# Performance work log

Measured on AMD Instinct MI355X. Metric: run time of the kernel, lower is better.

## Reference

```python
import jax, jax.numpy as jnp
import numpy as np

# Static configuration (mirrors init_kwargs)
B, C, H, W = 4, 256, 128, 128
S, T = 512, 64          # style_dim, num style tokens
HC, HS = 4, 8           # cross-attn heads, spatial-attn heads
WS, G = 8, 4            # window size, groupnorm groups
SHARPEN = 2.0
EPS = 1e-5


def _ln(x, g, b):
    m = jnp.mean(x, -1, keepdims=True)
    v = jnp.var(x, -1, keepdims=True)
    return (x - m) * jax.lax.rsqrt(v + EPS) * g + b


def _sdpa(q, k, v, scale):
    # q,k,v: [B, nH, L, D]
    s = jnp.einsum('bhqd,bhkd->bhqk', q, k) * scale
    return jnp.einsum('bhqk,bhkd->bhqd', jax.nn.softmax(s, -1), v)


def _heads(t, nh):
    b, l, c = t.shape
    return t.reshape(b, l, nh, c // nh).transpose(0, 2, 1, 3)


def _unheads(t):
    b, nh, l, d = t.shape
    return t.transpose(0, 2, 1, 3).reshape(b, l, nh * d)


def setup_inputs() -> dict:
    key = jax.random.key(0)
    ks = iter(jax.random.split(key, 48))
    def w(shape, s=0.02):
        return jax.random.normal(next(ks), shape, jnp.float32) * s
    return {
        'x': jax.random.normal(next(ks), (B, C, H, W), jnp.float32),
        'style_code': jax.random.normal(next(ks), (B, S), jnp.float32),
        # SpatialSelfAttention params (1x1 convs == linear over channels)
        'qkv_w': w((3 * C, C)), 'spat_proj_w': w((C, C)),
        # CrossAttnAdaGN params
        'gproj_w': w((2 * C, S)),
        'gproj_b': jnp.concatenate([jnp.ones((C,), jnp.float32), jnp.zeros((C,), jnp.float32)]),
        'tokens_basis': w((T, C)),
        'sproj_w': w((C, S)), 'sproj_b': jnp.zeros((C,), jnp.float32),
        'pos_w1': w((C, 2)), 'pos_b1': jnp.zeros((C,), jnp.float32),
        'pos_w2': w((C, C)), 'pos_b2': jnp.zeros((C,), jnp.float32),
        'q_w': w((C, C)), 'q_b': jnp.zeros((C,), jnp.float32),
        'k_w': w((C, C)), 'k_b': jnp.zeros((C,), jnp.float32),
        'v_w': w((C, C)), 'v_b': jnp.zeros((C,), jnp.float32),
        'o_w': w((C, C)), 'o_b': jnp.zeros((C,), jnp.float32),
        'ffn_w1': w((2 * C, C)), 'ffn_b1': jnp.zeros((2 * C,), jnp.float32),
        'ffn_w2': w((C, 2 * C)), 'ffn_b2': jnp.zeros((C,), jnp.float32),
        'tn_g': jnp.ones((C,), jnp.float32), 'tn_b': jnp.zeros((C,), jnp.float32),
        'qn_g': jnp.ones((C,), jnp.float32), 'qn_b': jnp.zeros((C,), jnp.float32),
        'fn_g': jnp.ones((C,), jnp.float32), 'fn_b': jnp.zeros((C,), jnp.float32),
        'gamma': w((1, C, 1, 1), 0.1),
    }


def reference(x, style_code, qkv_w, spat_proj_w, gproj_w, gproj_b, tokens_basis,
              sproj_w, sproj_b, pos_w1, pos_b1, pos_w2, pos_b2,
              q_w, q_b, k_w, k_b, v_w, v_b, o_w, o_b,
              ffn_w1, ffn_b1, ffn_w2, ffn_b2,
              tn_g, tn_b, qn_g, qn_b, fn_g, fn_b, gamma):
    b = x.shape[0]
    hw = H * W
    # ---------- CrossAttnAdaGN style modulation ----------
    xg = x.reshape(b, G, C // G, H, W)
    mu = jnp.mean(xg, (2, 3, 4), keepdims=True)
    var = jnp.var(xg, (2, 3, 4), keepdims=True)
    normalized = ((xg - mu) * jax.lax.rsqrt(var + EPS)).reshape(b, C, H, W)
    gp = style_code @ gproj_w.T + gproj_b           # [B, 2C]
    scale = gp[:, :C, None, None]
    shift = gp[:, C:, None, None]
    style_tokens = tokens_basis[None] + (style_code @ sproj_w.T + sproj_b)[:, None]  # [B,T,C]
    style_tokens = _ln(style_tokens, tn_g, tn_b)
    gy = jnp.linspace(-1.0, 1.0, H)
    gx = jnp.linspace(-1.0, 1.0, W)
    grid_y, grid_x = jnp.meshgrid(gy, gx, indexing='ij')
    pos = jnp.stack([grid_x, grid_y], -1).reshape(hw, 2)                 # [HW,2]
    pos_emb = jax.nn.silu(pos @ pos_w1.T + pos_b1) @ pos_w2.T + pos_b2   # [HW,C]
    tok = normalized.transpose(0, 2, 3, 1).reshape(b, hw, C)
    q_in = _ln(tok + pos_emb[None], qn_g, qn_b)
    q = _heads(q_in @ q_w.T + q_b, HC)                 # [B,HC,HW,hd]
    k = _heads(style_tokens @ k_w.T + k_b, HC)         # [B,HC,T,hd]
    v = _heads(style_tokens @ v_w.T + v_b, HC)
    hd = C // HC
    sc = _unheads(_sdpa(q, k, v, SHARPEN / jnp.sqrt(jnp.float32(hd))))   # [B,HW,C]
    sc = sc @ o_w.T + o_b
    sc = sc + jax.nn.silu(_ln(sc, fn_g, fn_b) @ ffn_w1.T + ffn_b1) @ ffn_w2.T + ffn_b2
    sc_sp = sc.transpose(0, 2, 1).reshape(b, C, H, W)
    adagn = normalized * scale + shift + sc_sp * gamma
    h = x + adagn  # gate = 1.0, residual style modulation
    # ---------- shifted-window self-attention ----------
    sh = WS // 2
    xr = jnp.roll(h, (-sh, -sh), (2, 3))
    qkv = jnp.einsum('oi,bihw->bohw', qkv_w, xr)
    qs, ks_, vs = jnp.split(qkv, 3, axis=1)
    def win(t):  # [B,C,H,W] -> [B*nWin, WS*WS, C]
        return t.reshape(b, C, H // WS, WS, W // WS, WS).transpose(0, 2, 4, 3, 5, 1).reshape(-1, WS * WS, C)
    hd2 = C // HS
    qh = _heads(win(qs), HS)
    kh = _heads(win(ks_), HS)
    vh = _heads(win(vs), HS)
    out = _unheads(_sdpa(qh, kh, vh, 1.0 / jnp.sqrt(jnp.float32(hd2))))
    out = out.reshape(b, H // WS, W // WS, WS, WS, C).transpose(0, 5, 1, 3, 2, 4).reshape(b, C, H, W)
    out = jnp.roll(out, (sh, sh), (2, 3))
    out = jnp.einsum('oi,bihw->bohw', spat_proj_w, out)
    return h + out
```

## Files before the change

### kernel.cpp

```cpp
#include <hip/hip_runtime.h>
#include <stdint.h>

#define DEV __device__ __forceinline__

typedef unsigned short u16;
typedef unsigned int u32;
typedef __attribute__((ext_vector_type(8))) __bf16 bf16x8;
typedef __attribute__((ext_vector_type(4))) float f32x4;

DEV u16 f2b(float f) {
  u32 u = __float_as_uint(f);
  u32 r = (u + 0x7FFFu + ((u >> 16) & 1u)) >> 16;
  return (u16)r;
}
DEV float b2f(u16 u) { return __uint_as_float(((u32)u) << 16); }
DEV void up2(u32 u, float& a, float& b) {
  a = __uint_as_float(u << 16);
  b = __uint_as_float(u & 0xffff0000u);
}
DEV void up8(uint4 t, float* d) {
  up2(t.x, d[0], d[1]); up2(t.y, d[2], d[3]);
  up2(t.z, d[4], d[5]); up2(t.w, d[6], d[7]);
}
DEV float silu_f(float v) { return v / (1.0f + __expf(-v)); }

DEV float redmax16(float v) {
  v = fmaxf(v, __shfl_xor(v, 1));
  v = fmaxf(v, __shfl_xor(v, 2));
  v = fmaxf(v, __shfl_xor(v, 4));
  v = fmaxf(v, __shfl_xor(v, 8));
  return v;
}
DEV float redsum16(float v) {
  v += __shfl_xor(v, 1);
  v += __shfl_xor(v, 2);
  v += __shfl_xor(v, 4);
  v += __shfl_xor(v, 8);
  return v;
}

DEV void gload16(const u16* g, u16* l) {
  __builtin_amdgcn_global_load_lds(
      (const __attribute__((address_space(1))) uint32_t*)(g),
      (__attribute__((address_space(3))) uint32_t*)(l), 16, 0, 0);
}

struct WConv {
  const float* s0; const float* s1; const float* s2; const float* s3;
  const float* s4; const float* s5; const float* s6;
  u16* d0; u16* d1; u16* d2; u16* d3; u16* d4; u16* d5; u16* d6;
};
__global__ void k_conv_all(WConv wc) {
  int i = blockIdx.x * 256 + threadIdx.x;
  if (i >= 180224) return;
  const float* sp[7] = {wc.s0, wc.s1, wc.s2, wc.s3, wc.s4, wc.s5, wc.s6};
  u16* dp[7] = {wc.d0, wc.d1, wc.d2, wc.d3, wc.d4, wc.d5, wc.d6};
  const int n4[7] = {16384, 16384, 32768, 32768, 49152, 16384, 16384};
  int rem = i, seg = 0;
#pragma unroll
  for (int s = 0; s < 7; ++s) {
    if (rem < n4[s]) { seg = s; break; }
    rem -= n4[s];
  }
  float4 v = ((const float4*)sp[seg])[rem];
  u16 t[4] = {f2b(v.x), f2b(v.y), f2b(v.z), f2b(v.w)};
  *(uint2*)(dp[seg] + (rem << 2)) = *(uint2*)t;
}

DEV void breduce2(float& a, float& b, float* red, int tid) {
#pragma unroll
  for (int off = 32; off > 0; off >>= 1) {
    a += __shfl_down(a, off);
    b += __shfl_down(b, off);
  }
  int lane = tid & 63, wv = tid >> 6;
  if (lane == 0) { red[wv * 2] = a; red[wv * 2 + 1] = b; }
  __syncthreads();
  a = red[0] + red[2] + red[4] + red[6];
  b = red[1] + red[3] + red[5] + red[7];
}

template <int XB>
__global__ void k_gn_partial(const float* __restrict__ x, float* __restrict__ partials,
                             u16* __restrict__ xb) {
  __shared__ float red[8];
  int chunk = blockIdx.x;
  size_t base4 = ((size_t)chunk) << 12;
  const float4* x4 = (const float4*)x;
  float a = 0.f, b = 0.f;
#pragma unroll 4
  for (int i = 0; i < 16; ++i) {
    size_t idx = base4 + (i << 8) + threadIdx.x;
    float4 v = x4[idx];
    a += v.x + v.y + v.z + v.w;
    b += v.x * v.x + v.y * v.y + v.z * v.z + v.w * v.w;
    if (XB) {
      u16 t[4] = {f2b(v.x), f2b(v.y), f2b(v.z), f2b(v.w)};
      *(uint2*)(xb + (idx << 2)) = *(uint2*)t;
    }
  }
  breduce2(a, b, red, threadIdx.x);
  if (threadIdx.x == 0) { partials[chunk * 2] = a; partials[chunk * 2 + 1] = b; }
}

__global__ void k_gn_final(const float* __restrict__ partials, float* __restrict__ stats) {
  int g = blockIdx.x, lane = threadIdx.x;
  float a = partials[(((g << 6) + lane) << 1)];
  float b = partials[(((g << 6) + lane) << 1) + 1];
#pragma unroll
  for (int off = 32; off > 0; off >>= 1) {
    a += __shfl_down(a, off);
    b += __shfl_down(b, off);
  }
  if (lane == 0) {
    float mean = a * (1.f / 1048576.f);
    float var = b * (1.f / 1048576.f) - mean * mean;
    stats[g << 1] = mean;
    stats[(g << 1) + 1] = rsqrtf(var + 1e-5f);
  }
}

__global__ void k_style(const float* __restrict__ sc, const float* __restrict__ gw,
                        const float* __restrict__ gb, const float* __restrict__ sw,
                        const float* __restrict__ sb, float* __restrict__ gp,
                        float* __restrict__ stok) {
  __shared__ float row[512];
  int b = blockIdx.y, part = blockIdx.x, tid = threadIdx.x;
  row[tid] = sc[(b << 9) + tid];
  row[tid + 256] = sc[(b << 9) + tid + 256];
  __syncthreads();
  if (part < 2) {
    int o = (part << 8) + tid;
    float s = gb[o];
    const float* wr = gw + ((size_t)o << 9);
#pragma unroll 8
    for (int j = 0; j < 512; ++j) s += row[j] * wr[j];
    gp[(b << 9) + o] = s;
  } else {
    float s = sb[tid];
    const float* wr = sw + ((size_t)tid << 9);
#pragma unroll 8
    for (int j = 0; j < 512; ++j) s += row[j] * wr[j];
    stok[(b << 8) + tid] = s;
  }
}

__global__ void k_styk(const float* __restrict__ tb, const float* __restrict__ stok,
                       const float* __restrict__ g, const float* __restrict__ bt,
                       float* __restrict__ styk) {
  __shared__ float red[8];
  int r = blockIdx.x;
  int b = r >> 6, t = r & 63;
  int c = threadIdx.x;
  float v = tb[(t << 8) + c] + stok[(b << 8) + c];
  float a = v, bb = v * v;
  breduce2(a, bb, red, c);
  float mean = a * (1.f / 256.f);
  float var = bb * (1.f / 256.f) - mean * mean;
  float rs = rsqrtf(var + 1e-5f);
  styk[((size_t)r << 8) + c] = (v - mean) * rs * g[c] + bt[c];
}

__global__ void k_kv(const float* __restrict__ styk, const float* __restrict__ kw,
                     const float* __restrict__ kb, const float* __restrict__ vw,
                     const float* __restrict__ vb, u16* __restrict__ kmat,
                     u16* __restrict__ vmat) {
  __shared__ float srow[256];
  int r = blockIdx.x, c = threadIdx.x;
  srow[c] = styk[((size_t)r << 8) + c];
  __syncthreads();
  float sk = kb[c], sv = vb[c];
  const float* kr = kw + ((size_t)c << 8);
  const float* vr = vw + ((size_t)c << 8);
#pragma unroll 8
  for (int j = 0; j < 256; ++j) { sk += srow[j] * kr[j]; sv += srow[j] * vr[j]; }
  kmat[((size_t)r << 8) + c] = f2b(sk);
  vmat[((size_t)r << 8) + c] = f2b(sv);
}

__global__ void k_posh(const float* __restrict__ w1, const float* __restrict__ b1,
                       u16* __restrict__ posh) {
  int i = blockIdx.x * 256 + threadIdx.x;
  int stride = gridDim.x * 256;
  for (; i < 16384 * 256; i += stride) {
    int p = i >> 8, c = i & 255;
    int y = p >> 7, x = p & 127;
    float gx = -1.f + 2.f * (float)x / 127.f;
    float gy = -1.f + 2.f * (float)y / 127.f;
    float v = gx * w1[c << 1] + gy * w1[(c << 1) + 1] + b1[c];
    posh[i] = f2b(silu_f(v));
  }
}

template <int ACT, int BIAS, int RES, int SPLIT>
__global__ __launch_bounds__(256, 2) void k_gemm2(
    const u16* __restrict__ A, const u16* __restrict__ Bw,
    const float* __restrict__ bias, const u16* __restrict__ res,
    u16* __restrict__ o0, u16* __restrict__ o1, u16* __restrict__ o2,
    int M, int N, int K) {
  __shared__ __align__(16) u16 lds[17408];
  u16* sA = lds;
  u16* sB = lds + 4096;
  const int tid = threadIdx.x;
  const int lane = tid & 63, wv = tid >> 6;
  const int m0 = blockIdx.y << 7, n0 = blockIdx.x << 7;
  const int l15 = lane & 15, lg = lane >> 4;
  const int wr = wv >> 1, wc = wv & 1;

  const int gofs = (((lane & 3) ^ ((lane >> 3) & 3)) << 3);
  const int lrow = lane >> 2;
  const u16* Ag0 = A + (size_t)(m0 + (wv << 5) + lrow) * K + gofs;
  const u16* Ag1 = A + (size_t)(m0 + (wv << 5) + 16 + lrow) * K + gofs;
  const u16* Bg0 = Bw + (size_t)(n0 + (wv << 5) + lrow) * K + gofs;
  const u16* Bg1 = Bw + (size_t)(n0 + (wv << 5) + 16 + lrow) * K + gofs;
  u16* lA0 = sA + (wv << 10);
  u16* lA1 = sA + (wv << 10) + 512;
  u16* lB0 = sB + (wv << 10);
  u16* lB1 = sB + (wv << 10) + 512;

  const int roff = l15 * 32 + (((lg ^ ((l15 >> 1) & 3))) << 3);
  const int abase = (wr << 6) * 32;
  const int bbase = (wc << 6) * 32;

  f32x4 acc[4][4];
  f32x4 zz = {0.f, 0.f, 0.f, 0.f};
#pragma unroll
  for (int mi = 0; mi < 4; ++mi)
#pragma unroll
    for (int ni = 0; ni < 4; ++ni) acc[mi][ni] = zz;

  for (int kt = 0; kt < K; kt += 32) {
    __syncthreads();
    gload16(Ag0 + kt, lA0);
    gload16(Ag1 + kt, lA1);
    gload16(Bg0 + kt, lB0);
    gload16(Bg1 + kt, lB1);
    __syncthreads();
    bf16x8 af[4], bfv[4];
#pragma unroll
    for (int mi = 0; mi < 4; ++mi) af[mi] = *(const bf16x8*)&sA[abase + mi * 512 + roff];
#pragma unroll
    for (int ni = 0; ni < 4; ++ni) bfv[ni] = *(const bf16x8*)&sB[bbase + ni * 512 + roff];
#pragma unroll
    for (int mi = 0; mi < 4; ++mi)
#pragma unroll
      for (int ni = 0; ni < 4; ++ni)
        acc[mi][ni] = __builtin_amdgcn_mfma_f32_16x16x32_bf16(af[mi], bfv[ni], acc[mi][ni], 0, 0, 0);
  }

  float bv[4];
#pragma unroll
  for (int ni = 0; ni < 4; ++ni)
    bv[ni] = BIAS ? bias[n0 + (wc << 6) + (ni << 4) + l15] : 0.0f;
  __syncthreads();
  const int lg4 = lg << 2;
#pragma unroll
  for (int mi = 0; mi < 4; ++mi) {
#pragma unroll
    for (int ni = 0; ni < 4; ++ni) {
#pragma unroll
      for (int r = 0; r < 4; ++r) {
        int row = (wr << 6) + (mi << 4) + lg4 + r;
        int col = (wc << 6) + (ni << 4) + l15;
        float v = acc[mi][ni][r] + bv[ni];
        if (ACT == 1) v = silu_f(v);
        lds[row * 136 + col] = f2b(v);
      }
    }
  }
  __syncthreads();
  u16* obase;
  int cb, ldc;
  if (SPLIT) {
    int sel = n0 >> 8;
    obase = sel == 0 ? o0 : (sel == 1 ? o1 : o2);
    cb = n0 & 255;
    ldc = 256;
  } else {
    obase = o0;
    cb = n0;
    ldc = N;
  }
#pragma unroll
  for (int i = 0; i < 8; ++i) {
    int flat = (i << 8) + tid;
    int row = flat >> 4, c8 = (flat & 15) << 3;
    uint4 vv = *(const uint4*)&lds[row * 136 + c8];
    size_t oi = (size_t)(m0 + row) * ldc + cb + c8;
    if (RES) {
      uint4 rr = *(const uint4*)(res + oi);
      float a8[8], r8[8];
      up8(vv, a8);
      up8(rr, r8);
      u16 t[8];
#pragma unroll
      for (int e = 0; e < 8; ++e) t[e] = f2b(a8[e] + r8[e]);
      vv = *(const uint4*)t;
    }
    *(uint4*)(obase + oi) = vv;
  }
}

template <int XB>
__global__ void k_tokpe(const float* __restrict__ x, const u16* __restrict__ xb,
                        const float* __restrict__ stats, const u16* __restrict__ pe,
                        u16* __restrict__ tokq) {
  __shared__ float lds[64][65];
  int p0 = blockIdx.x << 6, c0 = blockIdx.y << 6, b = blockIdx.z;
  int tid = threadIdx.x;
#pragma unroll
  for (int i = 0; i < 16; ++i) {
    int flat = (i << 8) + tid;
    int ci = flat >> 6, pi = flat & 63;
    int cch = c0 + ci;
    int g = (b << 2) + (cch >> 6);
    float mu = stats[g << 1], rs = stats[(g << 1) + 1];
    size_t idx = (((size_t)(b << 8) + cch) << 14) + p0 + pi;
    float xv = XB ? b2f(xb[idx]) : x[idx];
    lds[ci][pi] = (xv - mu) * rs;
  }
  __syncthreads();
#pragma unroll
  for (int i = 0; i < 16; ++i) {
    int flat = (i << 8) + tid;
    int pi = flat >> 6, ci = flat & 63;
    size_t row = (size_t)((b << 14) + p0 + pi);
    tokq[(row << 8) + c0 + ci] =
        f2b(lds[ci][pi] + b2f(pe[((size_t)(p0 + pi) << 8) + c0 + ci]));
  }
}

__global__ __launch_bounds__(256) void k_rowln8(const u16* __restrict__ in,
                                                const float* __restrict__ g,
                                                const float* __restrict__ bt,
                                                u16* __restrict__ out) {
  __shared__ float gs[256], bs[256];
  int tid = threadIdx.x;
  gs[tid] = g[tid];
  bs[tid] = bt[tid];
  __syncthreads();
  size_t base = (((size_t)(blockIdx.x << 5) + (tid >> 3)) << 8) + ((tid & 7) << 5);
  float v[32];
#pragma unroll
  for (int q = 0; q < 4; ++q) up8(*(const uint4*)(in + base + (q << 3)), &v[q << 3]);
  float a = 0.f, b = 0.f;
#pragma unroll
  for (int j = 0; j < 32; ++j) { a += v[j]; b += v[j] * v[j]; }
#pragma unroll
  for (int m = 1; m <= 4; m <<= 1) { a += __shfl_xor(a, m); b += __shfl_xor(b, m); }
  float mean = a * (1.f / 256.f);
  float var = b * (1.f / 256.f) - mean * mean;
  float rs = rsqrtf(var + 1e-5f);
  int c0 = (tid & 7) << 5;
#pragma unroll
  for (int q = 0; q < 4; ++q) {
    u16 tmp[8];
#pragma unroll
    for (int e = 0; e < 8; ++e) {
      int j = (q << 3) + e;
      tmp[e] = f2b((v[j] - mean) * rs * gs[c0 + j] + bs[c0 + j]);
    }
    *(uint4*)(out + base + (q << 3)) = *(uint4*)tmp;
  }
}

__global__ __launch_bounds__(256, 2) void k_cross_mfma(
    const u16* __restrict__ qmat, const u16* __restrict__ kmat,
    const u16* __restrict__ vmat, u16* __restrict__ attn_out) {
  __shared__ u16 Kl[64 * 72];
  __shared__ u16 Vt[64 * 72];
  __shared__ u16 Pl[4][64 * 72];
  const int tid = threadIdx.x;
  const int lane = tid & 63, wv = tid >> 6;
  const int l15 = lane & 15, lg = lane >> 4;
  const int b = blockIdx.z, h = blockIdx.y;
  const int q0 = blockIdx.x << 8;
  for (int c = tid; c < 512; c += 256) {
    int t = c >> 3, dg = (c & 7) << 3;
    size_t src = (((size_t)(b << 6) + t) << 8) + (h << 6) + dg;
    *(uint4*)&Kl[t * 72 + dg] = *(const uint4*)(kmat + src);
    uint4 vv = *(const uint4*)(vmat + src);
    const u16* pv = (const u16*)&vv;
#pragma unroll
    for (int e = 0; e < 8; ++e) Vt[(dg + e) * 72 + t] = pv[e];
  }
  __syncthreads();
  const size_t qrow0 = (size_t)(b << 14) + q0 + (wv << 6);
  f32x4 acc[4][4];
  f32x4 zz = {0.f, 0.f, 0.f, 0.f};
#pragma unroll
  for (int mi = 0; mi < 4; ++mi)
#pragma unroll
    for (int ni = 0; ni < 4; ++ni) acc[mi][ni] = zz;
#pragma unroll
  for (int ks = 0; ks < 2; ++ks) {
    bf16x8 a[4], bbf[4];
#pragma unroll
    for (int mi = 0; mi < 4; ++mi)
      a[mi] = *(const bf16x8*)(qmat + ((qrow0 + (mi << 4) + l15) << 8) + (h << 6) +
                               (ks << 5) + (lg << 3));
#pragma unroll
    for (int ni = 0; ni < 4; ++ni)
      bbf[ni] = *(const bf16x8*)&Kl[((ni << 4) + l15) * 72 + (ks << 5) + (lg << 3)];
#pragma unroll
    for (int mi = 0; mi < 4; ++mi)
#pragma unroll
      for (int ni = 0; ni < 4; ++ni)
        acc[mi][ni] = __builtin_amdgcn_mfma_f32_16x16x32_bf16(a[mi], bbf[ni], acc[mi][ni], 0, 0, 0);
  }
  const float SC = 0.25f;
#pragma unroll
  for (int mi = 0; mi < 4; ++mi) {
#pragma unroll
    for (int r = 0; r < 4; ++r) {
      float rm = acc[mi][0][r];
#pragma unroll
      for (int ni = 1; ni < 4; ++ni) rm = fmaxf(rm, acc[mi][ni][r]);
      rm = redmax16(rm);
      float pv[4];
      float rs = 0.f;
#pragma unroll
      for (int ni = 0; ni < 4; ++ni) {
        pv[ni] = __expf((acc[mi][ni][r] - rm) * SC);
        rs += pv[ni];
      }
      rs = redsum16(rs);
      float inv = 1.f / rs;
      int row = (mi << 4) + (lg << 2) + r;
#pragma unroll
      for (int ni = 0; ni < 4; ++ni)
        Pl[wv][row * 72 + (ni << 4) + l15] = f2b(pv[ni] * inv);
    }
  }
  __syncthreads();
  f32x4 o[4][4];
#pragma unroll
  for (int mi = 0; mi < 4; ++mi)
#pragma unroll
    for (int ni = 0; ni < 4; ++ni) o[mi][ni] = zz;
#pragma unroll
  for (int ks = 0; ks < 2; ++ks) {
    bf16x8 a[4], bbf[4];
#pragma unroll
    for (int mi = 0; mi < 4; ++mi)
      a[mi] = *(const bf16x8*)&Pl[wv][((mi << 4) + l15) * 72 + (ks << 5) + (lg << 3)];
#pragma unroll
    for (int ni = 0; ni < 4; ++ni)
      bbf[ni] = *(const bf16x8*)&Vt[((ni << 4) + l15) * 72 + (ks << 5) + (lg << 3)];
#pragma unroll
    for (int mi = 0; mi < 4; ++mi)
#pragma unroll
      for (int ni = 0; ni < 4; ++ni)
        o[mi][ni] = __builtin_amdgcn_mfma_f32_16x16x32_bf16(a[mi], bbf[ni], o[mi][ni], 0, 0, 0);
  }
  __syncthreads();
#pragma unroll
  for (int mi = 0; mi < 4; ++mi)
#pragma unroll
    for (int ni = 0; ni < 4; ++ni)
#pragma unroll
      for (int r = 0; r < 4; ++r)
        Pl[wv][((mi << 4) + (lg << 2) + r) * 72 + (ni << 4) + l15] = f2b(o[mi][ni][r]);
  __syncthreads();
  const int l8r = lane >> 3, l8c = lane & 7;
#pragma unroll
  for (int it = 0; it < 8; ++it) {
    int row = (it << 3) + l8r;
    uint4 vv = *(const uint4*)&Pl[wv][row * 72 + (l8c << 3)];
    *(uint4*)(attn_out + ((qrow0 + row) << 8) + (h << 6) + (l8c << 3)) = vv;
  }
}

__global__ __launch_bounds__(256, 2) void k_win_mfma(
    const u16* __restrict__ qb, const u16* __restrict__ kbuf,
    const u16* __restrict__ vbuf, u16* __restrict__ wout) {
  __shared__ u16 Vt[4][32 * 72];
  __shared__ u16 Pl[4][64 * 72];
  const int tid = threadIdx.x;
  const int lane = tid & 63, wv = tid >> 6;
  const int l15 = lane & 15, lg = lane >> 4;
  const int win = blockIdx.x, b = blockIdx.y;
  const int wbase = ((win >> 4) << 10) + ((win & 15) << 3);
  const size_t bbase = (size_t)b << 14;
  const float SC = 0.17677669529663687f;
  f32x4 zz = {0.f, 0.f, 0.f, 0.f};
#pragma unroll 1
  for (int h2 = 0; h2 < 2; ++h2) {
    const int h = (wv << 1) + h2;
    const int co = h << 5;
    {
      int p = wbase + ((lane >> 3) << 7) + (lane & 7);
      const u16* src = vbuf + ((bbase + p) << 8) + co;
#pragma unroll
      for (int c = 0; c < 4; ++c) {
        uint4 vv = *(const uint4*)(src + (c << 3));
        const u16* pe = (const u16*)&vv;
#pragma unroll
        for (int e = 0; e < 8; ++e) Vt[wv][((c << 3) + e) * 72 + lane] = pe[e];
      }
    }
    f32x4 acc[4][4];
#pragma unroll
    for (int mi = 0; mi < 4; ++mi)
#pragma unroll
      for (int ni = 0; ni < 4; ++ni) acc[mi][ni] = zz;
    {
      bf16x8 a[4], bbf[4];
#pragma unroll
      for (int mi = 0; mi < 4; ++mi) {
        int t = (mi << 4) + l15;
        int p = wbase + ((t >> 3) << 7) + (t & 7);
        a[mi] = *(const bf16x8*)(qb + ((bbase + p) << 8) + co + (lg << 3));
      }
#pragma unroll
      for (int ni = 0; ni < 4; ++ni) {
        int t = (ni << 4) + l15;
        int p = wbase + ((t >> 3) << 7) + (t & 7);
        bbf[ni] = *(const bf16x8*)(kbuf + ((bbase + p) << 8) + co + (lg << 3));
      }
#pragma unroll
      for (int mi = 0; mi < 4; ++mi)
#pragma unroll
        for (int ni = 0; ni < 4; ++ni)
          acc[mi][ni] = __builtin_amdgcn_mfma_f32_16x16x32_bf16(a[mi], bbf[ni], acc[mi][ni], 0, 0, 0);
    }
#pragma unroll
    for (int mi = 0; mi < 4; ++mi) {
#pragma unroll
      for (int r = 0; r < 4; ++r) {
        float rm = acc[mi][0][r];
#pragma unroll
        for (int ni = 1; ni < 4; ++ni) rm = fmaxf(rm, acc[mi][ni][r]);
        rm = redmax16(rm);
        float pv[4];
        float rs = 0.f;
#pragma unroll
        for (int ni = 0; ni < 4; ++ni) {
          pv[ni] = __expf((acc[mi][ni][r] - rm) * SC);
          rs += pv[ni];
        }
        rs = redsum16(rs);
        float inv = 1.f / rs;
        int row = (mi << 4) + (lg << 2) + r;
#pragma unroll
        for (int ni = 0; ni < 4; ++ni)
          Pl[wv][row * 72 + (ni << 4) + l15] = f2b(pv[ni] * inv);
      }
    }
    __syncthreads();
    f32x4 o[4][2];
#pragma unroll
    for (int mi = 0; mi < 4; ++mi)
#pragma unroll
      for (int ni = 0; ni < 2; ++ni) o[mi][ni] = zz;
#pragma unroll
    for (int ks = 0; ks < 2; ++ks) {
      bf16x8 a[4], bbf[2];
#pragma unroll
      for (int mi = 0; mi < 4; ++mi)
        a[mi] = *(const bf16x8*)&Pl[wv][((mi << 4) + l15) * 72 + (ks << 5) + (lg << 3)];
#pragma unroll
      for (int ni = 0; ni < 2; ++ni)
        bbf[ni] = *(const bf16x8*)&Vt[wv][((ni << 4) + l15) * 72 + (ks << 5) + (lg << 3)];
#pragma unroll
      for (int mi = 0; mi < 4; ++mi)
#pragma unroll
        for (int ni = 0; ni < 2; ++ni)
          o[mi][ni] = __builtin_amdgcn_mfma_f32_16x16x32_bf16(a[mi], bbf[ni], o[mi][ni], 0, 0, 0);
    }
    __syncthreads();
#pragma unroll
    for (int mi = 0; mi < 4; ++mi)
#pragma unroll
      for (int ni = 0; ni < 2; ++ni)
#pragma unroll
        for (int r = 0; r < 4; ++r)
          Pl[wv][((mi << 4) + (lg << 2) + r) * 72 + (ni << 4) + l15] = f2b(o[mi][ni][r]);
    __syncthreads();
#pragma unroll
    for (int it = 0; it < 4; ++it) {
      int row = (it << 4) + (lane >> 2);
      int cg = (lane & 3) << 3;
      uint4 vv = *(const uint4*)&Pl[wv][row * 72 + cg];
      int p = wbase + ((row >> 3) << 7) + (row & 7);
      *(uint4*)(wout + ((bbase + p) << 8) + co + cg) = vv;
    }
    __syncthreads();
  }
}

template <int XB>
__global__ void k_xrt(const float* __restrict__ x, const u16* __restrict__ xb,
                      const u16* __restrict__ sc2, const float* __restrict__ stats,
                      const float* __restrict__ gp, const float* __restrict__ gamma,
                      u16* __restrict__ xrt) {
  __shared__ float A[64][33];
  __shared__ float Bt[32][65];
  int p0 = blockIdx.x << 6, c0 = blockIdx.y << 5, b = blockIdx.z;
  int tid = threadIdx.x;
#pragma unroll
  for (int i = 0; i < 8; ++i) {
    int flat = (i << 8) + tid;
    int pi = flat >> 5, ci = flat & 31;
    A[pi][ci] = b2f(sc2[(((size_t)(b << 14) + p0 + pi) << 8) + c0 + ci]);
  }
  __syncthreads();
#pragma unroll
  for (int i = 0; i < 8; ++i) {
    int flat = (i << 8) + tid;
    int cc = flat >> 6, px = flat & 63;
    int cch = c0 + cc;
    int g = (b << 2) + (cch >> 6);
    float mu = stats[g << 1], rs = stats[(g << 1) + 1];
    size_t xi = (((size_t)(b << 8) + cch) << 14) + p0 + px;
    float xv = XB ? b2f(xb[xi]) : x[xi];
    float val = xv + (xv - mu) * rs * gp[(b << 9) + cch] + gp[(b << 9) + 256 + cch] +
                A[px][cc] * gamma[cch];
    Bt[cc][px] = val;
  }
  __syncthreads();
#pragma unroll
  for (int i = 0; i < 8; ++i) {
    int flat = (i << 8) + tid;
    int xi2 = flat >> 5, ci = flat & 31;
    int p = p0 + xi2;
    int yy = p >> 7, xx = p & 127;
    int pr = (((yy + 124) & 127) << 7) + ((xx + 124) & 127);
    xrt[(((size_t)(b << 14) + pr) << 8) + c0 + ci] = f2b(Bt[ci][xi2]);
  }
}

template <int XB>
__global__ void k_final(const float* __restrict__ x, const u16* __restrict__ xb,
                        const u16* __restrict__ sc2, const u16* __restrict__ out2,
                        const float* __restrict__ stats, const float* __restrict__ gp,
                        const float* __restrict__ gamma, float* __restrict__ dout) {
  __shared__ float L1[64][33];
  __shared__ float L2[64][33];
  int bx = blockIdx.x;
  int y = bx >> 1, x0 = (bx & 1) << 6;
  int c0 = blockIdx.y << 5, b = blockIdx.z;
  int tid = threadIdx.x;
#pragma unroll
  for (int i = 0; i < 8; ++i) {
    int flat = (i << 8) + tid;
    int xi = flat >> 5, ci = flat & 31;
    int xx = x0 + xi;
    int pr = (((y + 124) & 127) << 7) + ((xx + 124) & 127);
    L1[xi][ci] = b2f(out2[(((size_t)(b << 14) + pr) << 8) + c0 + ci]);
    L2[xi][ci] = b2f(sc2[(((size_t)(b << 14) + (y << 7) + xx) << 8) + c0 + ci]);
  }
  __syncthreads();
#pragma unroll
  for (int i = 0; i < 8; ++i) {
    int flat = (i << 8) + tid;
    int cc = flat >> 6, xi2 = flat & 63;
    int cch = c0 + cc;
    int g = (b << 2) + (cch >> 6);
    float mu = stats[g << 1], rs = stats[(g << 1) + 1];
    size_t idx = (((size_t)(b << 8) + cch) << 14) + (y << 7) + x0 + xi2;
    float xv = XB ? b2f(xb[idx]) : x[idx];
    float val = xv + (xv - mu) * rs * gp[(b << 9) + cch] + gp[(b << 9) + 256 + cch] +
                L2[xi2][cc] * gamma[cch] + L1[xi2][cc];
    dout[idx] = val;
  }
}

extern "C" void kernel_launch(void* const* d_in, const int* in_sizes, int n_in,
                              void* d_out, int out_size, void* d_ws, size_t ws_size,
                              hipStream_t stream) {
  (void)in_sizes; (void)n_in; (void)out_size;
  const float* x = (const float*)d_in[0];
  const float* style = (const float*)d_in[1];
  const float* qkv_w = (const float*)d_in[2];
  const float* spat_w = (const float*)d_in[3];
  const float* gproj_w = (const float*)d_in[4];
  const float* gproj_b = (const float*)d_in[5];
  const float* tokens_basis = (const float*)d_in[6];
  const float* sproj_w = (const float*)d_in[7];
  const float* sproj_b = (const float*)d_in[8];
  const float* pos_w1 = (const float*)d_in[9];
  const float* pos_b1 = (const float*)d_in[10];
  const float* pos_w2 = (const float*)d_in[11];
  const float* pos_b2 = (const float*)d_in[12];
  const float* q_w = (const float*)d_in[13];
  const float* q_b = (const float*)d_in[14];
  const float* k_w = (const float*)d_in[15];
  const float* k_b = (const float*)d_in[16];
  const float* v_w = (const float*)d_in[17];
  const float* v_b = (const float*)d_in[18];
  const float* o_w = (const float*)d_in[19];
  const float* o_b = (const float*)d_in[20];
  const float* ffn_w1 = (const float*)d_in[21];
  const float* ffn_b1 = (const float*)d_in[22];
  const float* ffn_w2 = (const float*)d_in[23];
  const float* ffn_b2 = (const float*)d_in[24];
  const float* tn_g = (const float*)d_in[25];
  const float* tn_b = (const float*)d_in[26];
  const float* qn_g = (const float*)d_in[27];
  const float* qn_b = (const float*)d_in[28];
  const float* fn_g = (const float*)d_in[29];
  const float* fn_b = (const float*)d_in[30];
  const float* gamma = (const float*)d_in[31];
  float* dout = (float*)d_out;

  char* w = (char*)d_ws;
  size_t off = 0;
  auto alloc = [&](size_t sz) {
    char* p = w + off;
    off += (sz + 255) & ~(size_t)255;
    return (void*)p;
  };
  float* partials = (float*)alloc(1024 * 2 * 4);
  float* stats = (float*)alloc(32 * 4);
  float* gp = (float*)alloc(4 * 512 * 4);
  float* stok = (float*)alloc(4 * 256 * 4);
  float* styk = (float*)alloc(4 * 64 * 256 * 4);
  u16* kmat = (u16*)alloc(4 * 64 * 256 * 2);
  u16* vmat = (u16*)alloc(4 * 64 * 256 * 2);
  u16* wb_q = (u16*)alloc(65536 * 2);
  u16* wb_o = (u16*)alloc(65536 * 2);
  u16* wb_w1 = (u16*)alloc(131072 * 2);
  u16* wb_w2 = (u16*)alloc(131072 * 2);
  u16* wb_qkv = (u16*)alloc(196608 * 2);
  u16* wb_sp = (u16*)alloc(65536 * 2);
  u16* wb_p2 = (u16*)alloc(65536 * 2);
  const size_t SLOT = (size_t)65536 * 256 * 2;
  u16* S0 = (u16*)alloc(SLOT);
  u16* S1 = (u16*)alloc(SLOT);
  u16* S2 = (u16*)alloc(SLOT);
  size_t off_base = off;
  u16* xb = (u16*)alloc((size_t)67108864 * 2);
  if (ws_size < off_base) return;
  const int XB = (ws_size >= off) ? 1 : 0;

  u16* ffn_h = (u16*)d_out;
  u16* kwin = (u16*)d_out;
  u16* vwin = (u16*)d_out + (size_t)65536 * 256;

  WConv wc = {q_w, o_w, ffn_w1, ffn_w2, qkv_w, spat_w, pos_w2,
              wb_q, wb_o, wb_w1, wb_w2, wb_qkv, wb_sp, wb_p2};
  k_conv_all<<<704, 256, 0, stream>>>(wc);

  if (XB) k_gn_partial<1><<<1024, 256, 0, stream>>>(x, partials, xb);
  else k_gn_partial<0><<<1024, 256, 0, stream>>>(x, partials, xb);
  k_gn_final<<<16, 64, 0, stream>>>(partials, stats);

  k_style<<<dim3(3, 4), 256, 0, stream>>>(style, gproj_w, gproj_b, sproj_w, sproj_b, gp, stok);
  k_styk<<<256, 256, 0, stream>>>(tokens_basis, stok, tn_g, tn_b, styk);
  k_kv<<<256, 256, 0, stream>>>(styk, k_w, k_b, v_w, v_b, kmat, vmat);

  k_posh<<<4096, 256, 0, stream>>>(pos_w1, pos_b1, S0);
  k_gemm2<0, 1, 0, 0><<<dim3(2, 128), 256, 0, stream>>>(S0, wb_p2, pos_b2, nullptr,
                                                        S1, nullptr, nullptr, 16384, 256, 256);

  if (XB) k_tokpe<1><<<dim3(256, 4, 4), 256, 0, stream>>>(x, xb, stats, S1, S2);
  else k_tokpe<0><<<dim3(256, 4, 4), 256, 0, stream>>>(x, xb, stats, S1, S2);
  k_rowln8<<<2048, 256, 0, stream>>>(S2, qn_g, qn_b, S2);

  k_gemm2<0, 1, 0, 0><<<dim3(2, 512), 256, 0, stream>>>(S2, wb_q, q_b, nullptr,
                                                        S1, nullptr, nullptr, 65536, 256, 256);
  k_cross_mfma<<<dim3(64, 4, 4), 256, 0, stream>>>(S1, kmat, vmat, S0);
  k_gemm2<0, 1, 0, 0><<<dim3(2, 512), 256, 0, stream>>>(S0, wb_o, o_b, nullptr,
                                                        S2, nullptr, nullptr, 65536, 256, 256);

  k_rowln8<<<2048, 256, 0, stream>>>(S2, fn_g, fn_b, S1);
  k_gemm2<1, 1, 0, 0><<<dim3(4, 512), 256, 0, stream>>>(S1, wb_w1, ffn_b1, nullptr,
                                                        ffn_h, nullptr, nullptr, 65536, 512, 256);
  k_gemm2<0, 1, 1, 0><<<dim3(2, 512), 256, 0, stream>>>(ffn_h, wb_w2, ffn_b2, S2,
                                                        S0, nullptr, nullptr, 65536, 256, 512);

  if (XB) k_xrt<1><<<dim3(256, 8, 4), 256, 0, stream>>>(x, xb, S0, stats, gp, gamma, S1);
  else k_xrt<0><<<dim3(256, 8, 4), 256, 0, stream>>>(x, xb, S0, stats, gp, gamma, S1);

  k_gemm2<0, 0, 0, 1><<<dim3(6, 512), 256, 0, stream>>>(S1, wb_qkv, nullptr, nullptr,
                                                        S2, kwin, vwin, 65536, 768, 256);

  k_win_mfma<<<dim3(256, 4), 256, 0, stream>>>(S2, kwin, vwin, S1);
  k_gemm2<0, 0, 0, 0><<<dim3(2, 512), 256, 0, stream>>>(S1, wb_sp, nullptr, nullptr,
                                                        S2, nullptr, nullptr, 65536, 256, 256);

  if (XB) k_final<1><<<dim3(256, 8, 4), 256, 0, stream>>>(x, xb, S0, S2, stats, gp, gamma, dout);
  else k_final<0><<<dim3(256, 8, 4), 256, 0, stream>>>(x, xb, S0, S2, stats, gp, gamma, dout);
}
```

Before: 449.0 us.

## Fuse token LN into tokpe, remap GEMM blocks per XCD, reuse shifted h in final

The token normalisation plus positional-embedding kernel now also performs the query LayerNorm in one pass, removing a separate row-LN kernel and a round trip through memory. The GEMM block index is remapped so consecutive M-tiles land on the same XCD, aiming for better L2 reuse of the weight and A tiles. The final kernel reuses the already-computed rolled residual h (stored in bf16 for the QKV GEMM) instead of recomputing the AdaGN expression from x, stats and style parameters. That saves reads but makes the residual in the output bf16-rounded, and tokpe2 holds 64 floats per thread in registers.

```diff
diff --git a/kernel.cpp b/kernel.cpp
--- a/kernel.cpp
+++ b/kernel.cpp
@@ -203,7 +203,13 @@
   u16* sB = lds + 4096;
   const int tid = threadIdx.x;
   const int lane = tid & 63, wv = tid >> 6;
-  const int m0 = blockIdx.y << 7, n0 = blockIdx.x << 7;
+  const int nx = gridDim.x;
+  const int L = blockIdx.x + nx * blockIdx.y;
+  const int xcd = L & 7;
+  const int t = L >> 3;
+  const int nblk = t % nx;
+  const int mblk = ((t / nx) << 3) + xcd;
+  const int m0 = mblk << 7, n0 = nblk << 7;
   const int l15 = lane & 15, lg = lane >> 4;
   const int wr = wv >> 1, wc = wv & 1;
 
@@ -292,41 +298,82 @@
       float a8[8], r8[8];
       up8(vv, a8);
       up8(rr, r8);
-      u16 t[8];
-#pragma unroll
-      for (int e = 0; e < 8; ++e) t[e] = f2b(a8[e] + r8[e]);
-      vv = *(const uint4*)t;
+      u16 t8[8];
+#pragma unroll
+      for (int e = 0; e < 8; ++e) t8[e] = f2b(a8[e] + r8[e]);
+      vv = *(const uint4*)t8;
     }
     *(uint4*)(obase + oi) = vv;
   }
 }
 
 template <int XB>
-__global__ void k_tokpe(const float* __restrict__ x, const u16* __restrict__ xb,
-                        const float* __restrict__ stats, const u16* __restrict__ pe,
-                        u16* __restrict__ tokq) {
-  __shared__ float lds[64][65];
-  int p0 = blockIdx.x << 6, c0 = blockIdx.y << 6, b = blockIdx.z;
-  int tid = threadIdx.x;
-#pragma unroll
-  for (int i = 0; i < 16; ++i) {
-    int flat = (i << 8) + tid;
-    int ci = flat >> 6, pi = flat & 63;
-    int cch = c0 + ci;
-    int g = (b << 2) + (cch >> 6);
-    float mu = stats[g << 1], rs = stats[(g << 1) + 1];
-    size_t idx = (((size_t)(b << 8) + cch) << 14) + p0 + pi;
-    float xv = XB ? b2f(xb[idx]) : x[idx];
-    lds[ci][pi] = (xv - mu) * rs;
-  }
-  __syncthreads();
-#pragma unroll
-  for (int i = 0; i < 16; ++i) {
-    int flat = (i << 8) + tid;
-    int pi = flat >> 6, ci = flat & 63;
-    size_t row = (size_t)((b << 14) + p0 + pi);
-    tokq[(row << 8) + c0 + ci] =
-        f2b(lds[ci][pi] + b2f(pe[((size_t)(p0 + pi) << 8) + c0 + ci]));
+__global__ __launch_bounds__(256) void k_tokpe2(
+    const float* __restrict__ x, const u16* __restrict__ xb,
+    const float* __restrict__ stats, const u16* __restrict__ pe,
+    const float* __restrict__ qg, const float* __restrict__ qb2,
+    u16* __restrict__ tokq) {
+  __shared__ u16 T[256 * 72];
+  __shared__ float red[64][8];
+  const int tid = threadIdx.x;
+  const int p0 = blockIdx.x << 6, b = blockIdx.y;
+  {
+    const int c = tid;
+    const int g = (b << 2) + (c >> 6);
+    const float mu = stats[g << 1], rs = stats[(g << 1) + 1];
+    const size_t base = (((size_t)(b << 8) + c) << 14) + p0;
+#pragma unroll
+    for (int j8 = 0; j8 < 8; ++j8) {
+      float f[8];
+      if (XB) {
+        up8(*(const uint4*)(xb + base + (j8 << 3)), f);
+      } else {
+        float4 v0 = *(const float4*)(x + base + (j8 << 3));
+        float4 v1 = *(const float4*)(x + base + (j8 << 3) + 4);
+        f[0] = v0.x; f[1] = v0.y; f[2] = v0.z; f[3] = v0.w;
+        f[4] = v1.x; f[5] = v1.y; f[6] = v1.z; f[7] = v1.w;
+      }
+      u16 t8[8];
+#pragma unroll
+      for (int e = 0; e < 8; ++e) t8[e] = f2b((f[e] - mu) * rs);
+      *(uint4*)&T[c * 72 + (j8 << 3)] = *(uint4*)t8;
+    }
+  }
+  __syncthreads();
+  const int p = tid & 63, cq = tid >> 6;
+  const size_t pebase = (((size_t)(p0 + p)) << 8) + (cq << 6);
+  float vbuf[64];
+  float a = 0.f, s = 0.f;
+#pragma unroll
+  for (int q = 0; q < 8; ++q) {
+    float pf[8];
+    up8(*(const uint4*)(pe + pebase + (q << 3)), pf);
+#pragma unroll
+    for (int e = 0; e < 8; ++e) {
+      int j = (q << 3) + e;
+      float v = b2f(T[((cq << 6) + j) * 72 + p]) + pf[e];
+      vbuf[j] = v;
+      a += v; s += v * v;
+    }
+  }
+  red[p][cq << 1] = a;
+  red[p][(cq << 1) + 1] = s;
+  __syncthreads();
+  float sa = red[p][0] + red[p][2] + red[p][4] + red[p][6];
+  float ss = red[p][1] + red[p][3] + red[p][5] + red[p][7];
+  float mean = sa * (1.f / 256.f);
+  float var = ss * (1.f / 256.f) - mean * mean;
+  float rsg = rsqrtf(var + 1e-5f);
+  const size_t orow = (((size_t)(b << 14) + p0 + p) << 8) + (cq << 6);
+#pragma unroll
+  for (int q = 0; q < 8; ++q) {
+    u16 t8[8];
+#pragma unroll
+    for (int e = 0; e < 8; ++e) {
+      int j = (q << 3) + e;
+      t8[e] = f2b((vbuf[j] - mean) * rsg * qg[(cq << 6) + j] + qb2[(cq << 6) + j]);
+    }
+    *(uint4*)(tokq + orow + (q << 3)) = *(uint4*)t8;
   }
 }
 
@@ -630,13 +677,9 @@
   }
 }
 
-template <int XB>
-__global__ void k_final(const float* __restrict__ x, const u16* __restrict__ xb,
-                        const u16* __restrict__ sc2, const u16* __restrict__ out2,
-                        const float* __restrict__ stats, const float* __restrict__ gp,
-                        const float* __restrict__ gamma, float* __restrict__ dout) {
-  __shared__ float L1[64][33];
-  __shared__ float L2[64][33];
+__global__ void k_final2(const u16* __restrict__ xr, const u16* __restrict__ out2,
+                         float* __restrict__ dout) {
+  __shared__ float L[64][33];
   int bx = blockIdx.x;
   int y = bx >> 1, x0 = (bx & 1) << 6;
   int c0 = blockIdx.y << 5, b = blockIdx.z;
@@ -647,22 +690,16 @@
     int xi = flat >> 5, ci = flat & 31;
     int xx = x0 + xi;
     int pr = (((y + 124) & 127) << 7) + ((xx + 124) & 127);
-    L1[xi][ci] = b2f(out2[(((size_t)(b << 14) + pr) << 8) + c0 + ci]);
-    L2[xi][ci] = b2f(sc2[(((size_t)(b << 14) + (y << 7) + xx) << 8) + c0 + ci]);
+    size_t ii = (((size_t)(b << 14) + pr) << 8) + c0 + ci;
+    L[xi][ci] = b2f(xr[ii]) + b2f(out2[ii]);
   }
   __syncthreads();
 #pragma unroll
   for (int i = 0; i < 8; ++i) {
     int flat = (i << 8) + tid;
     int cc = flat >> 6, xi2 = flat & 63;
-    int cch = c0 + cc;
-    int g = (b << 2) + (cch >> 6);
-    float mu = stats[g << 1], rs = stats[(g << 1) + 1];
-    size_t idx = (((size_t)(b << 8) + cch) << 14) + (y << 7) + x0 + xi2;
-    float xv = XB ? b2f(xb[idx]) : x[idx];
-    float val = xv + (xv - mu) * rs * gp[(b << 9) + cch] + gp[(b << 9) + 256 + cch] +
-                L2[xi2][cc] * gamma[cch] + L1[xi2][cc];
-    dout[idx] = val;
+    size_t idx = (((size_t)(b << 8) + c0 + cc) << 14) + (y << 7) + x0 + xi2;
+    dout[idx] = L[xi2][cc];
   }
 }
 
@@ -754,9 +791,8 @@
   k_gemm2<0, 1, 0, 0><<<dim3(2, 128), 256, 0, stream>>>(S0, wb_p2, pos_b2, nullptr,
                                                         S1, nullptr, nullptr, 16384, 256, 256);
 
-  if (XB) k_tokpe<1><<<dim3(256, 4, 4), 256, 0, stream>>>(x, xb, stats, S1, S2);
-  else k_tokpe<0><<<dim3(256, 4, 4), 256, 0, stream>>>(x, xb, stats, S1, S2);
-  k_rowln8<<<2048, 256, 0, stream>>>(S2, qn_g, qn_b, S2);
+  if (XB) k_tokpe2<1><<<dim3(256, 4), 256, 0, stream>>>(x, xb, stats, S1, qn_g, qn_b, S2);
+  else k_tokpe2<0><<<dim3(256, 4), 256, 0, stream>>>(x, xb, stats, S1, qn_g, qn_b, S2);
 
   k_gemm2<0, 1, 0, 0><<<dim3(2, 512), 256, 0, stream>>>(S2, wb_q, q_b, nullptr,
                                                         S1, nullptr, nullptr, 65536, 256, 256);
@@ -776,10 +812,9 @@
   k_gemm2<0, 0, 0, 1><<<dim3(6, 512), 256, 0, stream>>>(S1, wb_qkv, nullptr, nullptr,
                                                         S2, kwin, vwin, 65536, 768, 256);
 
-  k_win_mfma<<<dim3(256, 4), 256, 0, stream>>>(S2, kwin, vwin, S1);
-  k_gemm2<0, 0, 0, 0><<<dim3(2, 512), 256, 0, stream>>>(S1, wb_sp, nullptr, nullptr,
+  k_win_mfma<<<dim3(256, 4), 256, 0, stream>>>(S2, kwin, vwin, S0);
+  k_gemm2<0, 0, 0, 0><<<dim3(2, 512), 256, 0, stream>>>(S0, wb_sp, nullptr, nullptr,
                                                         S2, nullptr, nullptr, 65536, 256, 256);
 
-  if (XB) k_final<1><<<dim3(256, 8, 4), 256, 0, stream>>>(x, xb, S0, S2, stats, gp, gamma, dout);
-  else k_final<0><<<dim3(256, 8, 4), 256, 0, stream>>>(x, xb, S0, S2, stats, gp, gamma, dout);
-}
+  k_final2<<<dim3(256, 8, 4), 256, 0, stream>>>(S1, S2, dout);
+}
```

Result: faster. 420.3 us (-6.4%).
